# Performance work log

Measured on AMD Instinct MI355X. Metric: run time of the kernel, lower is better.

Reference implementation:

```python
import jax, jax.numpy as jnp
import numpy as np

S, H = 8192, 2048

def setup_inputs() -> dict:
    key = jax.random.key(0)
    k1, k2, k3 = jax.random.split(key, 3)
    hidden = jax.random.normal(k1, (1, H), dtype=jnp.float32)
    encoder_outputs = jax.random.normal(k2, (S, 1, H), dtype=jnp.float32)
    W = jax.random.normal(k3, (H, H), dtype=jnp.float32) * (1.0 / np.sqrt(H))
    b = jnp.zeros((H,), dtype=jnp.float32)
    return {"hidden": hidden, "encoder_outputs": encoder_outputs, "W": W, "b": b}

def reference(hidden, encoder_outputs, W, b):
    # hidden: [1, H] -> [H]; encoder_outputs: [S, 1, H] -> [S, H]
    h = hidden[0]                      # [H]
    enc = encoder_outputs[:, 0, :]     # [S, H]
    # method='general': energy_i = h . (W @ enc_i + b)
    proj = jnp.einsum('sh,kh->sk', enc, W) + b   # [S, H] (Linear: x @ W.T + b)
    energies = proj @ h                          # [S]
    attn = jax.nn.softmax(energies, axis=0)      # softmax over seq dim
    return attn[None, None, :]                   # [1, 1, S]
```

## Files before the change

kernel.cpp:

```cpp
#include <hip/hip_runtime.h>


#define Hdim 2048
#define Sdim 8192

typedef float vfloat4 __attribute__((ext_vector_type(4)));

__global__ void kv_matvec(const float* __restrict__ W, const float* __restrict__ hid,
                          float* __restrict__ v) {
    int b = blockIdx.x;
    int c0 = (b & 7) * 256 + (b >> 3) * 8;
    int t = threadIdx.x;
    int cp = (t & 1) * 4;
    int rl = t >> 1;
    float4 acc = {0.f, 0.f, 0.f, 0.f};
#pragma unroll
    for (int i = 0; i < 8; ++i) {
        int k = rl + 256 * i;
        float hk = hid[k];
        float4 w = *reinterpret_cast<const float4*>(W + (size_t)k * Hdim + c0 + cp);
        acc.x += w.x * hk;
        acc.y += w.y * hk;
        acc.z += w.z * hk;
        acc.w += w.w * hk;
    }
    __shared__ float4 red[512];
    red[t] = acc;
    __syncthreads();
    for (int s = 128; s > 0; s >>= 1) {
        if (rl < s) {
            float4 o = red[t + 2 * s];
            float4 m = red[t];
            m.x += o.x; m.y += o.y; m.z += o.z; m.w += o.w;
            red[t] = m;
        }
        __syncthreads();
    }
    if (t < 2) *reinterpret_cast<float4*>(v + c0 + t * 4) = red[t];
}

__global__ __launch_bounds__(256) void k2_energies(
    const float* __restrict__ enc, const float* __restrict__ v, float* __restrict__ e) {
    __shared__ float v_lds[Hdim];
    int t = threadIdx.x;
    int lane = t & 63;
    int s = blockIdx.x * 4 + (t >> 6);
    {
        float4* dst = reinterpret_cast<float4*>(v_lds);
        const float4* src = reinterpret_cast<const float4*>(v);
        dst[t] = src[t];
        dst[t + 256] = src[t + 256];
    }
    const float* row = enc + (size_t)s * Hdim;
    vfloat4 a[8];
#pragma unroll
    for (int i = 0; i < 8; ++i)
        a[i] = __builtin_nontemporal_load(
            reinterpret_cast<const vfloat4*>(row + i * 256 + lane * 4));
    __syncthreads();
    float acc = 0.f;
#pragma unroll
    for (int i = 0; i < 8; ++i) {
        float4 w = *reinterpret_cast<float4*>(&v_lds[i * 256 + lane * 4]);
        acc += a[i].x * w.x + a[i].y * w.y + a[i].z * w.z + a[i].w * w.w;
    }
#pragma unroll
    for (int off = 32; off > 0; off >>= 1) acc += __shfl_xor(acc, off, 64);
    if (lane == 0) e[s] = acc;
}

__global__ void k3_par(const float* __restrict__ e, float* __restrict__ out) {
    __shared__ float red[4];
    __shared__ float bM, bL;
    int t = threadIdx.x, lane = t & 63, wv = t >> 6;
    float4 x[8];
#pragma unroll
    for (int i = 0; i < 8; ++i)
        x[i] = *reinterpret_cast<const float4*>(e + i * 1024 + t * 4);
    float m = x[0].x;
#pragma unroll
    for (int i = 0; i < 8; ++i) {
        m = fmaxf(m, fmaxf(fmaxf(x[i].x, x[i].y), fmaxf(x[i].z, x[i].w)));
    }
#pragma unroll
    for (int off = 32; off > 0; off >>= 1) m = fmaxf(m, __shfl_xor(m, off, 64));
    if (lane == 0) red[wv] = m;
    __syncthreads();
    if (t == 0) bM = fmaxf(fmaxf(red[0], red[1]), fmaxf(red[2], red[3]));
    __syncthreads();
    float M = bM;
    float l = 0.f;
#pragma unroll
    for (int i = 0; i < 8; ++i) {
        l += __expf(x[i].x - M) + __expf(x[i].y - M) +
             __expf(x[i].z - M) + __expf(x[i].w - M);
    }
#pragma unroll
    for (int off = 32; off > 0; off >>= 1) l += __shfl_xor(l, off, 64);
    __syncthreads();
    if (lane == 0) red[wv] = l;
    __syncthreads();
    if (t == 0) bL = red[0] + red[1] + red[2] + red[3];
    __syncthreads();
    float invL = 1.0f / bL;
    int idx = blockIdx.x * 256 + t;
    out[idx] = __expf(e[idx] - M) * invL;
}

extern "C" void kernel_launch(void* const* d_in, const int* in_sizes, int n_in,
                              void* d_out, int out_size, void* d_ws, size_t ws_size,
                              hipStream_t stream) {
    const float* hid = (const float*)d_in[0];
    const float* enc = (const float*)d_in[1];
    const float* W   = (const float*)d_in[2];
    float* out = (float*)d_out;
    float* ws = (float*)d_ws;

    float* v = ws;
    float* e = v + Hdim;

    kv_matvec<<<256, 512, 0, stream>>>(W, hid, v);
    k2_energies<<<Sdim / 4, 256, 0, stream>>>(enc, v, e);
    k3_par<<<32, 256, 0, stream>>>(e, out);
}
```

Before: 23.48 us.

## Process two rows per wave in energies kernel and use shuffle reduction in matvec

The energies kernel now has each wave handle two encoder rows, halving the grid. Each wave issues 16 outstanding vector loads before the shared v staging, which gives more memory-level parallelism and halves the per-row cost of the LDS fill. The W matvec replaces its log-step shared-memory tree reduction with wave shuffles plus a small 8-wave final sum, removing many barriers. More registers per thread may lower occupancy.

After: 24.87 us. 1.06x slower.

```diff
diff --git a/kernel.cpp b/kernel.cpp
--- a/kernel.cpp
+++ b/kernel.cpp
@@ -11,6 +11,7 @@
     int b = blockIdx.x;
     int c0 = (b & 7) * 256 + (b >> 3) * 8;
     int t = threadIdx.x;
+    int lane = t & 63, wv = t >> 6;
     int cp = (t & 1) * 4;
     int rl = t >> 1;
     float4 acc = {0.f, 0.f, 0.f, 0.f};
@@ -24,19 +25,25 @@
         acc.z += w.z * hk;
         acc.w += w.w * hk;
     }
-    __shared__ float4 red[512];
-    red[t] = acc;
+#pragma unroll
+    for (int off = 2; off <= 32; off <<= 1) {
+        acc.x += __shfl_xor(acc.x, off, 64);
+        acc.y += __shfl_xor(acc.y, off, 64);
+        acc.z += __shfl_xor(acc.z, off, 64);
+        acc.w += __shfl_xor(acc.w, off, 64);
+    }
+    __shared__ float4 wsum[8][2];
+    if (lane < 2) wsum[wv][lane] = acc;
     __syncthreads();
-    for (int s = 128; s > 0; s >>= 1) {
-        if (rl < s) {
-            float4 o = red[t + 2 * s];
-            float4 m = red[t];
-            m.x += o.x; m.y += o.y; m.z += o.z; m.w += o.w;
-            red[t] = m;
+    if (t < 2) {
+        float4 s = wsum[0][t];
+#pragma unroll
+        for (int w = 1; w < 8; ++w) {
+            float4 o = wsum[w][t];
+            s.x += o.x; s.y += o.y; s.z += o.z; s.w += o.w;
         }
-        __syncthreads();
+        *reinterpret_cast<float4*>(v + c0 + t * 4) = s;
     }
-    if (t < 2) *reinterpret_cast<float4*>(v + c0 + t * 4) = red[t];
 }
 
 __global__ __launch_bounds__(256) void k2_energies(
@@ -44,29 +51,41 @@
     __shared__ float v_lds[Hdim];
     int t = threadIdx.x;
     int lane = t & 63;
-    int s = blockIdx.x * 4 + (t >> 6);
+    size_t r0 = (size_t)blockIdx.x * 8 + (t >> 6) * 2;
+    const float* pA = enc + r0 * Hdim;
+    const float* pB = pA + Hdim;
+    vfloat4 a[8], bb[8];
+#pragma unroll
+    for (int i = 0; i < 8; ++i)
+        a[i] = __builtin_nontemporal_load(
+            reinterpret_cast<const vfloat4*>(pA + i * 256 + lane * 4));
+#pragma unroll
+    for (int i = 0; i < 8; ++i)
+        bb[i] = __builtin_nontemporal_load(
+            reinterpret_cast<const vfloat4*>(pB + i * 256 + lane * 4));
     {
         float4* dst = reinterpret_cast<float4*>(v_lds);
         const float4* src = reinterpret_cast<const float4*>(v);
         dst[t] = src[t];
         dst[t + 256] = src[t + 256];
     }
-    const float* row = enc + (size_t)s * Hdim;
-    vfloat4 a[8];
-#pragma unroll
-    for (int i = 0; i < 8; ++i)
-        a[i] = __builtin_nontemporal_load(
-            reinterpret_cast<const vfloat4*>(row + i * 256 + lane * 4));
     __syncthreads();
-    float acc = 0.f;
+    float accA = 0.f, accB = 0.f;
 #pragma unroll
     for (int i = 0; i < 8; ++i) {
         float4 w = *reinterpret_cast<float4*>(&v_lds[i * 256 + lane * 4]);
-        acc += a[i].x * w.x + a[i].y * w.y + a[i].z * w.z + a[i].w * w.w;
+        accA += a[i].x * w.x + a[i].y * w.y + a[i].z * w.z + a[i].w * w.w;
+        accB += bb[i].x * w.x + bb[i].y * w.y + bb[i].z * w.z + bb[i].w * w.w;
     }
 #pragma unroll
-    for (int off = 32; off > 0; off >>= 1) acc += __shfl_xor(acc, off, 64);
-    if (lane == 0) e[s] = acc;
+    for (int off = 32; off > 0; off >>= 1) {
+        accA += __shfl_xor(accA, off, 64);
+        accB += __shfl_xor(accB, off, 64);
+    }
+    if (lane == 0) {
+        e[r0] = accA;
+        e[r0 + 1] = accB;
+    }
 }
 
 __global__ void k3_par(const float* __restrict__ e, float* __restrict__ out) {
@@ -120,6 +139,6 @@
     float* e = v + Hdim;
 
     kv_matvec<<<256, 512, 0, stream>>>(W, hid, v);
-    k2_energies<<<Sdim / 4, 256, 0, stream>>>(enc, v, e);
+    k2_energies<<<Sdim / 8, 256, 0, stream>>>(enc, v, e);
     k3_par<<<32, 256, 0, stream>>>(e, out);
 }
```
